# Kernel optimization log

Hardware: AMD Instinct MI355X
Metric: run time of the kernel (lower is better)

The kernel has to match this reference:

```python
import jax, jax.numpy as jnp
import numpy as np

N = 50000
E = 600000
D = 128


def setup_inputs() -> dict:
    key = jax.random.key(0)
    ks = jax.random.split(key, 10)
    scale = 1.0 / np.sqrt(D)
    inp = {
        "x": jax.random.normal(ks[0], (N, D), dtype=jnp.float32),
        "edge_index": jax.random.randint(ks[1], (2, E), 0, N, dtype=jnp.int64),
        # layer 0: fc + res_fc (residual=True, activation=relu)
        "W1": jax.random.normal(ks[2], (D, D), dtype=jnp.float32) * scale,
        "R1": jax.random.normal(ks[3], (D, D), dtype=jnp.float32) * scale,
        # layer 1
        "W2": jax.random.normal(ks[4], (D, D), dtype=jnp.float32) * scale,
        "R2": jax.random.normal(ks[5], (D, D), dtype=jnp.float32) * scale,
        # layer 2 (last, encoding=False -> no residual/activation)
        "W3": jax.random.normal(ks[6], (D, D), dtype=jnp.float32) * scale,
        # head Linear(out_dim, out_dim) with bias
        "Wh": jax.random.normal(ks[7], (D, D), dtype=jnp.float32) * scale,
        "bh": jnp.zeros((D,), dtype=jnp.float32),
    }
    return inp


def _gcn_stack(x, row, col, norm, W1, R1, W2, R2, W3, Wh, bh):
    n = x.shape[0]

    def conv(x, W, R, act):
        h = x @ W                                   # [N, D]
        msg = h[row] * norm[:, None]                # gather + per-edge scale [E+N, D]
        agg = jax.ops.segment_sum(msg, col, num_segments=n)  # scatter-add [N, D]
        if R is not None:
            agg = agg + x @ R                       # residual
        if act:
            agg = jax.nn.relu(agg)
        return agg

    x = conv(x, W1, R1, True)
    x = conv(x, W2, R2, True)
    x = conv(x, W3, None, False)
    return x @ Wh + bh


def reference(x, edge_index, W1, R1, W2, R2, W3, Wh, bh):
    n = x.shape[0]
    # add self loops (same edge structure for every layer)
    loops = jnp.arange(n, dtype=edge_index.dtype)
    row = jnp.concatenate([edge_index[0], loops])
    col = jnp.concatenate([edge_index[1], loops])
    # symmetric degree normalization: deg computed over col (incl. self loops)
    deg = jax.ops.segment_sum(jnp.ones_like(col, dtype=x.dtype), col, num_segments=n)
    dinv = deg ** -0.5
    norm = dinv[row] * dinv[col]                    # [E+N]
    return _gcn_stack(x, row, col, norm, W1, R1, W2, R2, W3, Wh, bh)
```

## Files before the change

kernel.cpp:

```cpp
#include <hip/hip_runtime.h>
#include <hip/hip_bf16.h>


#define SCAN_CHUNK 1024

typedef _Float16 half8 __attribute__((ext_vector_type(8)));
typedef _Float16 half4 __attribute__((ext_vector_type(4)));
typedef float floatx4 __attribute__((ext_vector_type(4)));

__global__ void zero_int_kernel(int* __restrict__ p, int n) {
    int i = blockIdx.x * blockDim.x + threadIdx.x;
    if (i < n) p[i] = 0;
}

__global__ void hist_kernel(const int* __restrict__ col, int* __restrict__ cnt, int E) {
    int i = blockIdx.x * blockDim.x + threadIdx.x;
    if (i < E) atomicAdd(&cnt[col[i]], 1);
}

__global__ void dinv_kernel(const int* __restrict__ cnt, float* __restrict__ dinv, int n) {
    int i = blockIdx.x * blockDim.x + threadIdx.x;
    if (i < n) dinv[i] = rsqrtf((float)(cnt[i] + 1));
}

__global__ __launch_bounds__(256) void scan_reduce_kernel(
        const int* __restrict__ cnt, int* __restrict__ bsum, int n) {
    __shared__ int s[256];
    int b = blockIdx.x, t = threadIdx.x;
    int base = b * SCAN_CHUNK + t * 4;
    int v = 0;
    if (base + 3 < n) {
        int4 q = *(const int4*)&cnt[base];
        v = q.x + q.y + q.z + q.w;
    } else {
        for (int i = 0; i < 4; ++i) if (base + i < n) v += cnt[base + i];
    }
    s[t] = v;
    __syncthreads();
    for (int off = 128; off > 0; off >>= 1) {
        if (t < off) s[t] += s[t + off];
        __syncthreads();
    }
    if (t == 0) bsum[b] = s[0];
}

__global__ __launch_bounds__(1024) void scan_bsum_kernel(
        const int* __restrict__ bsum, int* __restrict__ boff, int nb) {
    __shared__ int s[1024];
    int t = threadIdx.x;
    s[t] = (t < nb) ? bsum[t] : 0;
    __syncthreads();
    for (int off = 1; off < 1024; off <<= 1) {
        int add = (t >= off) ? s[t - off] : 0;
        __syncthreads();
        s[t] += add;
        __syncthreads();
    }
    if (t < nb) boff[t] = (t == 0) ? 0 : s[t - 1];
}

__global__ __launch_bounds__(256) void scan_write_kernel(
        const int* __restrict__ cnt, const int* __restrict__ boff,
        int* __restrict__ row_ptr, int* __restrict__ cursor, int n, int E) {
    __shared__ int s[256];
    int b = blockIdx.x, t = threadIdx.x;
    int base = b * SCAN_CHUNK + t * 4;
    int v[4];
    int sum = 0;
    for (int i = 0; i < 4; ++i) {
        v[i] = (base + i < n) ? cnt[base + i] : 0;
        sum += v[i];
    }
    s[t] = sum;
    __syncthreads();
    for (int off = 1; off < 256; off <<= 1) {
        int add = (t >= off) ? s[t - off] : 0;
        __syncthreads();
        s[t] += add;
        __syncthreads();
    }
    int prefix = boff[b] + ((t == 0) ? 0 : s[t - 1]);
    for (int i = 0; i < 4; ++i) {
        if (base + i < n) {
            row_ptr[base + i] = prefix;
            cursor[base + i] = prefix;
            prefix += v[i];
        }
    }
    if (b == 0 && t == 0) row_ptr[n] = E;
}

__global__ void fill_kernel(const int* __restrict__ row, const int* __restrict__ colv,
                            const float* __restrict__ dinv, int* __restrict__ cursor,
                            int2* __restrict__ csr, int E) {
    int i = blockIdx.x * blockDim.x + threadIdx.x;
    if (i < E) {
        int r = row[i], c = colv[i];
        int p = atomicAdd(&cursor[c], 1);
        float nrm = dinv[r] * dinv[c];
        csr[p] = make_int2(r, __float_as_int(nrm));
    }
}

__global__ __launch_bounds__(256) void wcvt_kernel(
        const float* __restrict__ W1, const float* __restrict__ R1,
        const float* __restrict__ W2, const float* __restrict__ R2,
        const float* __restrict__ W3, const float* __restrict__ Wh,
        _Float16* __restrict__ Wt) {
    __shared__ float tile[32][33];
    int b = blockIdx.x;
    int mat = b >> 4, tl = b & 15;
    const float* W = (mat == 0) ? W1 : (mat == 1) ? R1 : (mat == 2) ? W2
                   : (mat == 3) ? R2 : (mat == 4) ? W3 : Wh;
    _Float16* T = Wt + (size_t)mat * 16384;
    int tr = (tl >> 2) * 32, tc = (tl & 3) * 32;
    int t = threadIdx.x;
    int i = t >> 3, j4 = t & 7;
    float4 v = *(const float4*)&W[(tr + i) * 128 + tc + j4 * 4];
    tile[i][j4 * 4 + 0] = v.x;
    tile[i][j4 * 4 + 1] = v.y;
    tile[i][j4 * 4 + 2] = v.z;
    tile[i][j4 * 4 + 3] = v.w;
    __syncthreads();
    half4 h;
    h.x = (_Float16)tile[j4 * 4 + 0][i];
    h.y = (_Float16)tile[j4 * 4 + 1][i];
    h.z = (_Float16)tile[j4 * 4 + 2][i];
    h.w = (_Float16)tile[j4 * 4 + 3][i];
    *(half4*)&T[(tc + i) * 128 + tr + j4 * 4] = h;
}

template <int F32IN>
__global__ __launch_bounds__(256) void gemm_dual_kernel(
        const void* __restrict__ Xv, const _Float16* __restrict__ WtA,
        const _Float16* __restrict__ WtB, _Float16* __restrict__ outA,
        _Float16* __restrict__ outB, int n) {
    __shared__ _Float16 Af[64 * 136];
    __shared__ _Float16 Bt[128 * 136];
    int t = threadIdx.x;
    int r0 = blockIdx.x * 64;

    if (F32IN) {
        const float* X = (const float*)Xv;
#pragma unroll
        for (int i = 0; i < 8; ++i) {
            int flat = i * 256 + t;
            int r = flat >> 5, c4 = flat & 31;
            float4 v = make_float4(0.f, 0.f, 0.f, 0.f);
            if (r0 + r < n) v = ((const float4*)X)[(size_t)(r0 + r) * 32 + c4];
            half4 h;
            h.x = (_Float16)v.x; h.y = (_Float16)v.y;
            h.z = (_Float16)v.z; h.w = (_Float16)v.w;
            *(half4*)&Af[r * 136 + c4 * 4] = h;
        }
    } else {
        const _Float16* X = (const _Float16*)Xv;
#pragma unroll
        for (int i = 0; i < 4; ++i) {
            int flat = i * 256 + t;
            int r = flat >> 4, k8 = flat & 15;
            half8 v = {0, 0, 0, 0, 0, 0, 0, 0};
            if (r0 + r < n) v = *(const half8*)&X[(size_t)(r0 + r) * 128 + k8 * 8];
            *(half8*)&Af[r * 136 + k8 * 8] = v;
        }
    }
#pragma unroll
    for (int i = 0; i < 8; ++i) {
        int flat = i * 256 + t;
        int c = flat >> 4, k8 = flat & 15;
        *(half8*)&Bt[c * 136 + k8 * 8] = *(const half8*)&WtA[c * 128 + k8 * 8];
    }
    __syncthreads();

    int lane = t & 63, w = t >> 6;
    int m = lane & 15, q = lane >> 4;
    int rowb = r0 + w * 16 + q * 4;

    half8 a[4];
#pragma unroll
    for (int s = 0; s < 4; ++s)
        a[s] = *(const half8*)&Af[(w * 16 + m) * 136 + s * 32 + q * 8];

    floatx4 acc[8];
#pragma unroll
    for (int nt = 0; nt < 8; ++nt) acc[nt] = (floatx4){0.f, 0.f, 0.f, 0.f};
#pragma unroll
    for (int s = 0; s < 4; ++s)
#pragma unroll
        for (int nt = 0; nt < 8; ++nt) {
            half8 b = *(const half8*)&Bt[(nt * 16 + m) * 136 + s * 32 + q * 8];
            acc[nt] = __builtin_amdgcn_mfma_f32_16x16x32_f16(a[s], b, acc[nt], 0, 0, 0);
        }
    __syncthreads();
#pragma unroll
    for (int i = 0; i < 8; ++i) {
        int flat = i * 256 + t;
        int c = flat >> 4, k8 = flat & 15;
        *(half8*)&Bt[c * 136 + k8 * 8] = *(const half8*)&WtB[c * 128 + k8 * 8];
    }
#pragma unroll
    for (int nt = 0; nt < 8; ++nt) {
        int col = nt * 16 + m;
#pragma unroll
        for (int r = 0; r < 4; ++r) {
            int gr = rowb + r;
            if (gr < n) outA[(size_t)gr * 128 + col] = (_Float16)acc[nt][r];
        }
    }
    __syncthreads();

#pragma unroll
    for (int nt = 0; nt < 8; ++nt) acc[nt] = (floatx4){0.f, 0.f, 0.f, 0.f};
#pragma unroll
    for (int s = 0; s < 4; ++s)
#pragma unroll
        for (int nt = 0; nt < 8; ++nt) {
            half8 b = *(const half8*)&Bt[(nt * 16 + m) * 136 + s * 32 + q * 8];
            acc[nt] = __builtin_amdgcn_mfma_f32_16x16x32_f16(a[s], b, acc[nt], 0, 0, 0);
        }
#pragma unroll
    for (int nt = 0; nt < 8; ++nt) {
        int col = nt * 16 + m;
#pragma unroll
        for (int r = 0; r < 4; ++r) {
            int gr = rowb + r;
            if (gr < n) outB[(size_t)gr * 128 + col] = (_Float16)acc[nt][r];
        }
    }
}

__global__ __launch_bounds__(256) void gemm_h_kernel(
        const _Float16* __restrict__ X, const _Float16* __restrict__ Wt,
        _Float16* __restrict__ out, int n) {
    __shared__ _Float16 Af[64 * 136];
    __shared__ _Float16 Bt[128 * 136];
    int t = threadIdx.x;
    int r0 = blockIdx.x * 64;

#pragma unroll
    for (int i = 0; i < 4; ++i) {
        int flat = i * 256 + t;
        int r = flat >> 4, k8 = flat & 15;
        half8 v = {0, 0, 0, 0, 0, 0, 0, 0};
        if (r0 + r < n) v = *(const half8*)&X[(size_t)(r0 + r) * 128 + k8 * 8];
        *(half8*)&Af[r * 136 + k8 * 8] = v;
    }
#pragma unroll
    for (int i = 0; i < 8; ++i) {
        int flat = i * 256 + t;
        int c = flat >> 4, k8 = flat & 15;
        *(half8*)&Bt[c * 136 + k8 * 8] = *(const half8*)&Wt[c * 128 + k8 * 8];
    }
    __syncthreads();

    int lane = t & 63, w = t >> 6;
    int m = lane & 15, q = lane >> 4;

    floatx4 acc[8];
#pragma unroll
    for (int nt = 0; nt < 8; ++nt) acc[nt] = (floatx4){0.f, 0.f, 0.f, 0.f};

#pragma unroll
    for (int s = 0; s < 4; ++s) {
        half8 a = *(const half8*)&Af[(w * 16 + m) * 136 + s * 32 + q * 8];
#pragma unroll
        for (int nt = 0; nt < 8; ++nt) {
            half8 b = *(const half8*)&Bt[(nt * 16 + m) * 136 + s * 32 + q * 8];
            acc[nt] = __builtin_amdgcn_mfma_f32_16x16x32_f16(a, b, acc[nt], 0, 0, 0);
        }
    }

    int rowb = r0 + w * 16 + q * 4;
#pragma unroll
    for (int nt = 0; nt < 8; ++nt) {
        int col = nt * 16 + m;
#pragma unroll
        for (int r = 0; r < 4; ++r) {
            int gr = rowb + r;
            if (gr < n) out[(size_t)gr * 128 + col] = (_Float16)acc[nt][r];
        }
    }
}

__global__ __launch_bounds__(256) void gemm_f_kernel(
        const _Float16* __restrict__ X, const _Float16* __restrict__ Wt,
        const float* __restrict__ bias, float* __restrict__ out, int n) {
    __shared__ _Float16 Af[64 * 136];
    __shared__ _Float16 Bt[128 * 136];
    int t = threadIdx.x;
    int r0 = blockIdx.x * 64;

#pragma unroll
    for (int i = 0; i < 4; ++i) {
        int flat = i * 256 + t;
        int r = flat >> 4, k8 = flat & 15;
        half8 v = {0, 0, 0, 0, 0, 0, 0, 0};
        if (r0 + r < n) v = *(const half8*)&X[(size_t)(r0 + r) * 128 + k8 * 8];
        *(half8*)&Af[r * 136 + k8 * 8] = v;
    }
#pragma unroll
    for (int i = 0; i < 8; ++i) {
        int flat = i * 256 + t;
        int c = flat >> 4, k8 = flat & 15;
        *(half8*)&Bt[c * 136 + k8 * 8] = *(const half8*)&Wt[c * 128 + k8 * 8];
    }
    __syncthreads();

    int lane = t & 63, w = t >> 6;
    int m = lane & 15, q = lane >> 4;

    floatx4 acc[8];
#pragma unroll
    for (int nt = 0; nt < 8; ++nt) acc[nt] = (floatx4){0.f, 0.f, 0.f, 0.f};

#pragma unroll
    for (int s = 0; s < 4; ++s) {
        half8 a = *(const half8*)&Af[(w * 16 + m) * 136 + s * 32 + q * 8];
#pragma unroll
        for (int nt = 0; nt < 8; ++nt) {
            half8 b = *(const half8*)&Bt[(nt * 16 + m) * 136 + s * 32 + q * 8];
            acc[nt] = __builtin_amdgcn_mfma_f32_16x16x32_f16(a, b, acc[nt], 0, 0, 0);
        }
    }

    int rowb = r0 + w * 16 + q * 4;
#pragma unroll
    for (int nt = 0; nt < 8; ++nt) {
        int col = nt * 16 + m;
        float bb = bias[col];
#pragma unroll
        for (int r = 0; r < 4; ++r) {
            int gr = rowb + r;
            if (gr < n) out[(size_t)gr * 128 + col] = acc[nt][r] + bb;
        }
    }
}

__global__ void spmm_kernel(const _Float16* __restrict__ h, const _Float16* __restrict__ xr,
                            const int* __restrict__ row_ptr, const int2* __restrict__ csr,
                            const float* __restrict__ dinv, _Float16* __restrict__ out,
                            int n, int do_relu) {
    int gid = blockIdx.x * blockDim.x + threadIdx.x;
    int node = gid >> 6;
    int lane = gid & 63;
    if (node >= n) return;
    int sub = lane >> 4;
    int fl = lane & 15;
    const half8* hp8 = (const half8*)h;

    float acc[8];
#pragma unroll
    for (int j = 0; j < 8; ++j) acc[j] = 0.f;

    int e0 = row_ptr[node], e1 = row_ptr[node + 1];
    int e = e0;
    for (; e + 16 <= e1; e += 16) {
        int2 d0 = csr[e + sub];
        int2 d1 = csr[e + 4 + sub];
        int2 d2 = csr[e + 8 + sub];
        int2 d3 = csr[e + 12 + sub];
        half8 v0 = hp8[(size_t)d0.x * 16 + fl];
        half8 v1 = hp8[(size_t)d1.x * 16 + fl];
        half8 v2 = hp8[(size_t)d2.x * 16 + fl];
        half8 v3 = hp8[(size_t)d3.x * 16 + fl];
        float n0 = __int_as_float(d0.y), n1 = __int_as_float(d1.y);
        float n2 = __int_as_float(d2.y), n3 = __int_as_float(d3.y);
#pragma unroll
        for (int j = 0; j < 8; ++j) {
            acc[j] = fmaf(n0, (float)v0[j], acc[j]);
            acc[j] = fmaf(n1, (float)v1[j], acc[j]);
            acc[j] = fmaf(n2, (float)v2[j], acc[j]);
            acc[j] = fmaf(n3, (float)v3[j], acc[j]);
        }
    }
    for (; e < e1; e += 4) {
        int idx = e + sub;
        int act = idx < e1;
        int cidx = act ? idx : (e1 - 1);
        int2 d = csr[cidx];
        float nrm = act ? __int_as_float(d.y) : 0.f;
        half8 v = hp8[(size_t)d.x * 16 + fl];
#pragma unroll
        for (int j = 0; j < 8; ++j) acc[j] = fmaf(nrm, (float)v[j], acc[j]);
    }
#pragma unroll
    for (int j = 0; j < 8; ++j) {
        acc[j] += __shfl_xor(acc[j], 16, 64);
        acc[j] += __shfl_xor(acc[j], 32, 64);
    }

    float di = dinv[node];
    if (sub == 0) {
        float w = di * di;
        half8 hv = hp8[(size_t)node * 16 + fl];
#pragma unroll
        for (int j = 0; j < 8; ++j) acc[j] = fmaf(w, (float)hv[j], acc[j]);
        if (xr) {
            half8 r = ((const half8*)xr)[(size_t)node * 16 + fl];
#pragma unroll
            for (int j = 0; j < 8; ++j) acc[j] += (float)r[j];
        }
        if (do_relu) {
#pragma unroll
            for (int j = 0; j < 8; ++j) acc[j] = fmaxf(acc[j], 0.f);
        }
        half8 o;
#pragma unroll
        for (int j = 0; j < 8; ++j) o[j] = (_Float16)acc[j];
        ((half8*)out)[(size_t)node * 16 + fl] = o;
    }
}

extern "C" void kernel_launch(void* const* d_in, const int* in_sizes, int n_in,
                              void* d_out, int out_size, void* d_ws, size_t ws_size,
                              hipStream_t stream) {
    const float* x  = (const float*)d_in[0];
    const int*   ei = (const int*)d_in[1];
    const float* W1 = (const float*)d_in[2];
    const float* R1 = (const float*)d_in[3];
    const float* W2 = (const float*)d_in[4];
    const float* R2 = (const float*)d_in[5];
    const float* W3 = (const float*)d_in[6];
    const float* Wh = (const float*)d_in[7];
    const float* bh = (const float*)d_in[8];
    float* out = (float*)d_out;

    int N = in_sizes[0] / 128;
    int E = in_sizes[1] / 2;

    char* p = (char*)d_ws;
    auto alloc = [&](size_t bytes) {
        char* r = p;
        p += (bytes + 255) & ~(size_t)255;
        return r;
    };
    int*      cnt     = (int*)alloc((size_t)N * 4);
    int*      row_ptr = (int*)alloc((size_t)(N + 1) * 4);
    int*      cursor  = (int*)alloc((size_t)N * 4);
    float*    dinv    = (float*)alloc((size_t)N * 4);
    int*      bsum    = (int*)alloc((size_t)1024 * 4);
    int*      boff    = (int*)alloc((size_t)1024 * 4);
    int2*     csr     = (int2*)alloc((size_t)E * 8);
    _Float16* Wt      = (_Float16*)alloc((size_t)6 * 16384 * 2);
    _Float16* B0h     = (_Float16*)alloc((size_t)N * 128 * 2);
    _Float16* B1h     = (_Float16*)alloc((size_t)N * 128 * 2);
    _Float16* B2h     = (_Float16*)alloc((size_t)N * 128 * 2);

    const int* rowi = ei;
    const int* coli = ei + E;

    int nb = (N + SCAN_CHUNK - 1) / SCAN_CHUNK;

    zero_int_kernel<<<(N + 255) / 256, 256, 0, stream>>>(cnt, N);
    hist_kernel<<<(E + 255) / 256, 256, 0, stream>>>(coli, cnt, E);
    dinv_kernel<<<(N + 255) / 256, 256, 0, stream>>>(cnt, dinv, N);
    scan_reduce_kernel<<<nb, 256, 0, stream>>>(cnt, bsum, N);
    scan_bsum_kernel<<<1, 1024, 0, stream>>>(bsum, boff, nb);
    scan_write_kernel<<<nb, 256, 0, stream>>>(cnt, boff, row_ptr, cursor, N, E);
    fill_kernel<<<(E + 255) / 256, 256, 0, stream>>>(rowi, coli, dinv, cursor, csr, E);
    wcvt_kernel<<<96, 256, 0, stream>>>(W1, R1, W2, R2, W3, Wh, Wt);

    int gb = (N + 63) / 64;
    int sb = (N + 3) / 4;
    _Float16* Wt1 = Wt;
    _Float16* Rt1 = Wt + 16384;
    _Float16* Wt2 = Wt + 2 * 16384;
    _Float16* Rt2 = Wt + 3 * 16384;
    _Float16* Wt3 = Wt + 4 * 16384;
    _Float16* Wth = Wt + 5 * 16384;

    gemm_dual_kernel<1><<<gb, 256, 0, stream>>>(x, Wt1, Rt1, B0h, B1h, N);
    spmm_kernel<<<sb, 256, 0, stream>>>(B0h, B1h, row_ptr, csr, dinv, B1h, N, 1);
    gemm_dual_kernel<0><<<gb, 256, 0, stream>>>(B1h, Wt2, Rt2, B0h, B2h, N);
    spmm_kernel<<<sb, 256, 0, stream>>>(B0h, B2h, row_ptr, csr, dinv, B2h, N, 1);
    gemm_h_kernel<<<gb, 256, 0, stream>>>(B2h, Wt3, B0h, N);
    spmm_kernel<<<sb, 256, 0, stream>>>(B0h, nullptr, row_ptr, csr, dinv, B1h, N, 0);
    gemm_f_kernel<<<gb, 256, 0, stream>>>(B1h, Wth, bh, out, N);
}
```

Measured before the change: 317.2 us.

## Fold W3·Wh into one weight, fuse bias into final SpMM, merge dinv into scan

The last layer has no activation, so the product W3·Wh is precomputed into a single combined weight. The final SpMM then writes fp32 output with the bias added directly, which removes the separate head GEMM kernel and one N×128 round trip through memory. The dinv computation moves into scan_write_kernel, saving one launch. Reassociating the matmul and rounding the combined weight to fp16 changes numerics slightly.

```diff
diff --git a/kernel.cpp b/kernel.cpp
--- a/kernel.cpp
+++ b/kernel.cpp
@@ -16,11 +16,6 @@
 __global__ void hist_kernel(const int* __restrict__ col, int* __restrict__ cnt, int E) {
     int i = blockIdx.x * blockDim.x + threadIdx.x;
     if (i < E) atomicAdd(&cnt[col[i]], 1);
-}
-
-__global__ void dinv_kernel(const int* __restrict__ cnt, float* __restrict__ dinv, int n) {
-    int i = blockIdx.x * blockDim.x + threadIdx.x;
-    if (i < n) dinv[i] = rsqrtf((float)(cnt[i] + 1));
 }
 
 __global__ __launch_bounds__(256) void scan_reduce_kernel(
@@ -61,7 +56,8 @@
 
 __global__ __launch_bounds__(256) void scan_write_kernel(
         const int* __restrict__ cnt, const int* __restrict__ boff,
-        int* __restrict__ row_ptr, int* __restrict__ cursor, int n, int E) {
+        int* __restrict__ row_ptr, int* __restrict__ cursor,
+        float* __restrict__ dinv, int n, int E) {
     __shared__ int s[256];
     int b = blockIdx.x, t = threadIdx.x;
     int base = b * SCAN_CHUNK + t * 4;
@@ -84,6 +80,7 @@
         if (base + i < n) {
             row_ptr[base + i] = prefix;
             cursor[base + i] = prefix;
+            dinv[base + i] = rsqrtf((float)(v[i] + 1));
             prefix += v[i];
         }
     }
@@ -105,13 +102,11 @@
 __global__ __launch_bounds__(256) void wcvt_kernel(
         const float* __restrict__ W1, const float* __restrict__ R1,
         const float* __restrict__ W2, const float* __restrict__ R2,
-        const float* __restrict__ W3, const float* __restrict__ Wh,
         _Float16* __restrict__ Wt) {
     __shared__ float tile[32][33];
     int b = blockIdx.x;
     int mat = b >> 4, tl = b & 15;
-    const float* W = (mat == 0) ? W1 : (mat == 1) ? R1 : (mat == 2) ? W2
-                   : (mat == 3) ? R2 : (mat == 4) ? W3 : Wh;
+    const float* W = (mat == 0) ? W1 : (mat == 1) ? R1 : (mat == 2) ? W2 : R2;
     _Float16* T = Wt + (size_t)mat * 16384;
     int tr = (tl >> 2) * 32, tc = (tl & 3) * 32;
     int t = threadIdx.x;
@@ -130,6 +125,26 @@
     *(half4*)&T[(tc + i) * 128 + tr + j4 * 4] = h;
 }
 
+__global__ __launch_bounds__(256) void wc_kernel(
+        const float* __restrict__ W3, const float* __restrict__ Wh,
+        _Float16* __restrict__ Wtc) {
+    int b = blockIdx.x, t = threadIdx.x;
+    int c = b * 8 + (t >> 5);
+    int k0 = (t & 31) * 4;
+    float acc0 = 0.f, acc1 = 0.f, acc2 = 0.f, acc3 = 0.f;
+    for (int j = 0; j < 128; ++j) {
+        float wh = Wh[j * 128 + c];
+        acc0 = fmaf(W3[(k0 + 0) * 128 + j], wh, acc0);
+        acc1 = fmaf(W3[(k0 + 1) * 128 + j], wh, acc1);
+        acc2 = fmaf(W3[(k0 + 2) * 128 + j], wh, acc2);
+        acc3 = fmaf(W3[(k0 + 3) * 128 + j], wh, acc3);
+    }
+    half4 h;
+    h.x = (_Float16)acc0; h.y = (_Float16)acc1;
+    h.z = (_Float16)acc2; h.w = (_Float16)acc3;
+    *(half4*)&Wtc[c * 128 + k0] = h;
+}
+
 template <int F32IN>
 __global__ __launch_bounds__(256) void gemm_dual_kernel(
         const void* __restrict__ Xv, const _Float16* __restrict__ WtA,
@@ -282,64 +297,12 @@
     }
 }
 
-__global__ __launch_bounds__(256) void gemm_f_kernel(
-        const _Float16* __restrict__ X, const _Float16* __restrict__ Wt,
-        const float* __restrict__ bias, float* __restrict__ out, int n) {
-    __shared__ _Float16 Af[64 * 136];
-    __shared__ _Float16 Bt[128 * 136];
-    int t = threadIdx.x;
-    int r0 = blockIdx.x * 64;
-
-#pragma unroll
-    for (int i = 0; i < 4; ++i) {
-        int flat = i * 256 + t;
-        int r = flat >> 4, k8 = flat & 15;
-        half8 v = {0, 0, 0, 0, 0, 0, 0, 0};
-        if (r0 + r < n) v = *(const half8*)&X[(size_t)(r0 + r) * 128 + k8 * 8];
-        *(half8*)&Af[r * 136 + k8 * 8] = v;
-    }
-#pragma unroll
-    for (int i = 0; i < 8; ++i) {
-        int flat = i * 256 + t;
-        int c = flat >> 4, k8 = flat & 15;
-        *(half8*)&Bt[c * 136 + k8 * 8] = *(const half8*)&Wt[c * 128 + k8 * 8];
-    }
-    __syncthreads();
-
-    int lane = t & 63, w = t >> 6;
-    int m = lane & 15, q = lane >> 4;
-
-    floatx4 acc[8];
-#pragma unroll
-    for (int nt = 0; nt < 8; ++nt) acc[nt] = (floatx4){0.f, 0.f, 0.f, 0.f};
-
-#pragma unroll
-    for (int s = 0; s < 4; ++s) {
-        half8 a = *(const half8*)&Af[(w * 16 + m) * 136 + s * 32 + q * 8];
-#pragma unroll
-        for (int nt = 0; nt < 8; ++nt) {
-            half8 b = *(const half8*)&Bt[(nt * 16 + m) * 136 + s * 32 + q * 8];
-            acc[nt] = __builtin_amdgcn_mfma_f32_16x16x32_f16(a, b, acc[nt], 0, 0, 0);
-        }
-    }
-
-    int rowb = r0 + w * 16 + q * 4;
-#pragma unroll
-    for (int nt = 0; nt < 8; ++nt) {
-        int col = nt * 16 + m;
-        float bb = bias[col];
-#pragma unroll
-        for (int r = 0; r < 4; ++r) {
-            int gr = rowb + r;
-            if (gr < n) out[(size_t)gr * 128 + col] = acc[nt][r] + bb;
-        }
-    }
-}
-
+template <int RELU, int FINAL>
 __global__ void spmm_kernel(const _Float16* __restrict__ h, const _Float16* __restrict__ xr,
                             const int* __restrict__ row_ptr, const int2* __restrict__ csr,
-                            const float* __restrict__ dinv, _Float16* __restrict__ out,
-                            int n, int do_relu) {
+                            const float* __restrict__ dinv, _Float16* __restrict__ outh,
+                            float* __restrict__ outf, const float* __restrict__ bias,
+                            int n) {
     int gid = blockIdx.x * blockDim.x + threadIdx.x;
     int node = gid >> 6;
     int lane = gid & 63;
@@ -395,19 +358,30 @@
         half8 hv = hp8[(size_t)node * 16 + fl];
 #pragma unroll
         for (int j = 0; j < 8; ++j) acc[j] = fmaf(w, (float)hv[j], acc[j]);
-        if (xr) {
+        if (!FINAL && xr) {
             half8 r = ((const half8*)xr)[(size_t)node * 16 + fl];
 #pragma unroll
             for (int j = 0; j < 8; ++j) acc[j] += (float)r[j];
         }
-        if (do_relu) {
+        if (RELU) {
 #pragma unroll
             for (int j = 0; j < 8; ++j) acc[j] = fmaxf(acc[j], 0.f);
         }
-        half8 o;
-#pragma unroll
-        for (int j = 0; j < 8; ++j) o[j] = (_Float16)acc[j];
-        ((half8*)out)[(size_t)node * 16 + fl] = o;
+        if (FINAL) {
+            float4 b0 = *(const float4*)&bias[fl * 8];
+            float4 b1 = *(const float4*)&bias[fl * 8 + 4];
+            float4 o0 = make_float4(acc[0] + b0.x, acc[1] + b0.y,
+                                    acc[2] + b0.z, acc[3] + b0.w);
+            float4 o1 = make_float4(acc[4] + b1.x, acc[5] + b1.y,
+                                    acc[6] + b1.z, acc[7] + b1.w);
+            ((float4*)outf)[(size_t)node * 32 + fl * 2] = o0;
+            ((float4*)outf)[(size_t)node * 32 + fl * 2 + 1] = o1;
+        } else {
+            half8 o;
+#pragma unroll
+            for (int j = 0; j < 8; ++j) o[j] = (_Float16)acc[j];
+            ((half8*)outh)[(size_t)node * 16 + fl] = o;
+        }
     }
 }
 
@@ -441,7 +415,7 @@
     int*      bsum    = (int*)alloc((size_t)1024 * 4);
     int*      boff    = (int*)alloc((size_t)1024 * 4);
     int2*     csr     = (int2*)alloc((size_t)E * 8);
-    _Float16* Wt      = (_Float16*)alloc((size_t)6 * 16384 * 2);
+    _Float16* Wt      = (_Float16*)alloc((size_t)5 * 16384 * 2);
     _Float16* B0h     = (_Float16*)alloc((size_t)N * 128 * 2);
     _Float16* B1h     = (_Float16*)alloc((size_t)N * 128 * 2);
     _Float16* B2h     = (_Float16*)alloc((size_t)N * 128 * 2);
@@ -453,12 +427,12 @@
 
     zero_int_kernel<<<(N + 255) / 256, 256, 0, stream>>>(cnt, N);
     hist_kernel<<<(E + 255) / 256, 256, 0, stream>>>(coli, cnt, E);
-    dinv_kernel<<<(N + 255) / 256, 256, 0, stream>>>(cnt, dinv, N);
     scan_reduce_kernel<<<nb, 256, 0, stream>>>(cnt, bsum, N);
     scan_bsum_kernel<<<1, 1024, 0, stream>>>(bsum, boff, nb);
-    scan_write_kernel<<<nb, 256, 0, stream>>>(cnt, boff, row_ptr, cursor, N, E);
+    scan_write_kernel<<<nb, 256, 0, stream>>>(cnt, boff, row_ptr, cursor, dinv, N, E);
     fill_kernel<<<(E + 255) / 256, 256, 0, stream>>>(rowi, coli, dinv, cursor, csr, E);
-    wcvt_kernel<<<96, 256, 0, stream>>>(W1, R1, W2, R2, W3, Wh, Wt);
+    wcvt_kernel<<<64, 256, 0, stream>>>(W1, R1, W2, R2, Wt);
+    wc_kernel<<<16, 256, 0, stream>>>(W3, Wh, Wt + 4 * 16384);
 
     int gb = (N + 63) / 64;
     int sb = (N + 3) / 4;
@@ -466,14 +440,15 @@
     _Float16* Rt1 = Wt + 16384;
     _Float16* Wt2 = Wt + 2 * 16384;
     _Float16* Rt2 = Wt + 3 * 16384;
-    _Float16* Wt3 = Wt + 4 * 16384;
-    _Float16* Wth = Wt + 5 * 16384;
+    _Float16* Wtc = Wt + 4 * 16384;
 
     gemm_dual_kernel<1><<<gb, 256, 0, stream>>>(x, Wt1, Rt1, B0h, B1h, N);
-    spmm_kernel<<<sb, 256, 0, stream>>>(B0h, B1h, row_ptr, csr, dinv, B1h, N, 1);
+    spmm_kernel<1, 0><<<sb, 256, 0, stream>>>(B0h, B1h, row_ptr, csr, dinv,
+                                              B1h, nullptr, nullptr, N);
     gemm_dual_kernel<0><<<gb, 256, 0, stream>>>(B1h, Wt2, Rt2, B0h, B2h, N);
-    spmm_kernel<<<sb, 256, 0, stream>>>(B0h, B2h, row_ptr, csr, dinv, B2h, N, 1);
-    gemm_h_kernel<<<gb, 256, 0, stream>>>(B2h, Wt3, B0h, N);
-    spmm_kernel<<<sb, 256, 0, stream>>>(B0h, nullptr, row_ptr, csr, dinv, B1h, N, 0);
-    gemm_f_kernel<<<gb, 256, 0, stream>>>(B1h, Wth, bh, out, N);
-}
+    spmm_kernel<1, 0><<<sb, 256, 0, stream>>>(B0h, B2h, row_ptr, csr, dinv,
+                                              B2h, nullptr, nullptr, N);
+    gemm_h_kernel<<<gb, 256, 0, stream>>>(B2h, Wtc, B0h, N);
+    spmm_kernel<0, 1><<<sb, 256, 0, stream>>>(B0h, nullptr, row_ptr, csr, dinv,
+                                              nullptr, out, bh, N);
+}
```

New measurement: 315.7 us. Within noise of the previous version (-0.5%).
